# Kernel tuning notes

Hardware: AMD Instinct MI355X
Metric: run time of the kernel (lower is better)

The kernel has to match this reference:

```python
import jax, jax.numpy as jnp
import numpy as np

N_ATOMS = 50000
ATOM_FDIM = 133
HIDDEN = 128
DEPTH = 3
N_EDGES = 800000
N_MOLS = 1024
BN_EPS = 1e-5


def setup_inputs() -> dict:
    key = jax.random.key(0)
    ks = jax.random.split(key, 10)
    f_atoms = jax.random.normal(ks[0], (N_ATOMS, ATOM_FDIM), dtype=jnp.float32)
    W_in = jax.random.normal(ks[1], (ATOM_FDIM, HIDDEN), dtype=jnp.float32) / np.sqrt(ATOM_FDIM)
    b_in = jax.random.normal(ks[2], (HIDDEN,), dtype=jnp.float32) * 0.01
    W1 = jax.random.normal(ks[3], (DEPTH, HIDDEN, HIDDEN), dtype=jnp.float32) / np.sqrt(HIDDEN)
    b1 = jax.random.normal(ks[4], (DEPTH, HIDDEN), dtype=jnp.float32) * 0.01
    W2 = jax.random.normal(ks[5], (DEPTH, HIDDEN, HIDDEN), dtype=jnp.float32) / np.sqrt(HIDDEN)
    b2 = jax.random.normal(ks[6], (DEPTH, HIDDEN), dtype=jnp.float32) * 0.01
    gamma = jnp.ones((DEPTH, HIDDEN), dtype=jnp.float32)
    beta = jnp.zeros((DEPTH, HIDDEN), dtype=jnp.float32)
    eps_param = jnp.zeros((DEPTH,), dtype=jnp.float32)
    edge_index = jax.random.randint(ks[7], (2, N_EDGES), 0, N_ATOMS, dtype=jnp.int64 if jax.config.jax_enable_x64 else jnp.int32).astype(jnp.int32)
    segment_ids = jnp.sort(jax.random.randint(ks[8], (N_ATOMS,), 0, N_MOLS).astype(jnp.int32))
    return {"f_atoms": f_atoms, "W_in": W_in, "b_in": b_in, "W1": W1, "b1": b1,
            "W2": W2, "b2": b2, "gamma": gamma, "beta": beta, "eps_param": eps_param,
            "edge_index": edge_index, "segment_ids": segment_ids}


def _gin_forward(f_atoms, W_in, b_in, W1, b1, W2, b2, gamma, beta, eps_param,
                 edge_index, segment_ids):
    src, tgt = edge_index[0], edge_index[1]
    # input projection + ReLU
    x = jax.nn.relu(f_atoms @ W_in + b_in)  # [N, H]
    for d in range(DEPTH):
        # scatter-add of gathered neighbor features + (1+eps) self term
        agg = jnp.zeros_like(x).at[tgt].add(x[src]) + (1.0 + eps_param[d]) * x
        h = jax.nn.relu(agg @ W1[d] + b1[d])
        h = h @ W2[d] + b2[d]
        # BatchNorm1d (training-mode batch statistics)
        mean = jnp.mean(h, axis=0)
        var = jnp.var(h, axis=0)
        h = gamma[d] * (h - mean) * jax.lax.rsqrt(var + BN_EPS) + beta[d]
        x = jax.nn.relu(h)
    # per-molecule mean pooling (a_scope -> segment mean); empty mols -> zeros
    sums = jax.ops.segment_sum(x, segment_ids, num_segments=N_MOLS)  # [M, H]
    counts = jax.ops.segment_sum(jnp.ones((x.shape[0],), x.dtype), segment_ids,
                                 num_segments=N_MOLS)
    mol_vecs = jnp.where(counts[:, None] > 0, sums / jnp.maximum(counts, 1.0)[:, None], 0.0)
    return mol_vecs


def reference(f_atoms, W_in, b_in, W1, b1, W2, b2, gamma, beta, eps_param,
              edge_index, segment_ids):
    return _gin_forward(f_atoms, W_in, b_in, W1, b1, W2, b2, gamma, beta,
                        eps_param, edge_index, segment_ids)
```

## Files before the change

### kernel.cpp

```cpp
#include <hip/hip_runtime.h>
#include <hip/hip_fp16.h>

#define N_ATOMS   50000
#define ATOM_FDIM 133
#define HIDDEN    128
#define DEPTH     3
#define N_EDGES   800000
#define N_MOLS    1024
#define BN_EPS    1e-5f
#define K_IN_PAD  160

typedef _Float16 f16x8 __attribute__((ext_vector_type(8)));
typedef float    f32x4 __attribute__((ext_vector_type(4)));

struct __align__(8) half4pack { __half2 a, b; };

__global__ void hist_kernel(const int* __restrict__ idx, int n, int* __restrict__ cnt) {
    int i = blockIdx.x * blockDim.x + threadIdx.x;
    if (i < n) atomicAdd(&cnt[idx[i]], 1);
}

__global__ void scan_block_kernel(const int* __restrict__ in, int* __restrict__ out,
                                  int* __restrict__ bsum, int n) {
    __shared__ int buf[256];
    int i = blockIdx.x * 256 + threadIdx.x;
    int v = (i < n) ? in[i] : 0;
    buf[threadIdx.x] = v;
    __syncthreads();
    #pragma unroll
    for (int off = 1; off < 256; off <<= 1) {
        int t = (threadIdx.x >= off) ? buf[threadIdx.x - off] : 0;
        __syncthreads();
        buf[threadIdx.x] += t;
        __syncthreads();
    }
    if (i < n) out[i] = buf[threadIdx.x] - v;
    if (threadIdx.x == 255) bsum[blockIdx.x] = buf[255];
}

__global__ void scan_top_kernel(int* __restrict__ bsum, int nb) {
    __shared__ int buf[256];
    int v = (threadIdx.x < nb) ? bsum[threadIdx.x] : 0;
    buf[threadIdx.x] = v;
    __syncthreads();
    #pragma unroll
    for (int off = 1; off < 256; off <<= 1) {
        int t = (threadIdx.x >= off) ? buf[threadIdx.x - off] : 0;
        __syncthreads();
        buf[threadIdx.x] += t;
        __syncthreads();
    }
    if (threadIdx.x < nb) bsum[threadIdx.x] = buf[threadIdx.x] - v;
}

__global__ void scan_add_kernel(const int* __restrict__ partial, const int* __restrict__ bsum,
                                int* __restrict__ rowptr, int* __restrict__ wcur,
                                int n, int total) {
    int i = blockIdx.x * 256 + threadIdx.x;
    if (i < n) {
        int v = partial[i] + bsum[blockIdx.x];
        rowptr[i] = v;
        wcur[i]   = v;
    }
    if (i == 0) rowptr[n] = total;
}

__global__ void fill_csr_kernel(const int* __restrict__ src, const int* __restrict__ tgt,
                                int n, int* __restrict__ wcur, unsigned short* __restrict__ col) {
    int e = blockIdx.x * blockDim.x + threadIdx.x;
    if (e < n) {
        int t = tgt[e];
        int p = atomicAdd(&wcur[t], 1);
        col[p] = (unsigned short)src[e];
    }
}

__global__ void setup_kernel(const float* __restrict__ f,
                             const float* __restrict__ W_in,
                             const float* __restrict__ W1,
                             const float* __restrict__ W2,
                             const int* __restrict__ seg,
                             __half* __restrict__ Ah, __half* __restrict__ Wt,
                             float* __restrict__ stats, int* __restrict__ moloff)
{
    const int NCH = N_ATOMS * (K_IN_PAD / 4);
    const int NW4 = (128 * K_IN_PAD + 2 * DEPTH * 128 * 128) / 4;
    int i = blockIdx.x * 256 + threadIdx.x;
    if (i < NCH) {
        int row = i / (K_IN_PAD / 4);
        int c4  = (i - row * (K_IN_PAD / 4)) * 4;
        float v[4];
        #pragma unroll
        for (int u = 0; u < 4; ++u) {
            int k = c4 + u;
            v[u] = (k < ATOM_FDIM) ? f[(size_t)row * ATOM_FDIM + k] : 0.f;
        }
        half4pack p;
        p.a = __float22half2_rn(make_float2(v[0], v[1]));
        p.b = __float22half2_rn(make_float2(v[2], v[3]));
        *(half4pack*)&Ah[(size_t)row * K_IN_PAD + c4] = p;
        return;
    }
    int j = i - NCH;
    if (j < NW4) {
        float v[4];
        #pragma unroll
        for (int u = 0; u < 4; ++u) {
            int e = j * 4 + u;
            if (e < 128 * K_IN_PAD) {
                int n = e / K_IN_PAD, k = e - n * K_IN_PAD;
                v[u] = (k < ATOM_FDIM) ? W_in[(size_t)k * 128 + n] : 0.f;
            } else if (e < 128 * K_IN_PAD + DEPTH * 128 * 128) {
                int q = e - 128 * K_IN_PAD;
                int d = q >> 14, r = q & 16383;
                int n = r >> 7, k = r & 127;
                v[u] = W1[((size_t)d * 128 + k) * 128 + n];
            } else {
                int q = e - 128 * K_IN_PAD - DEPTH * 128 * 128;
                int d = q >> 14, r = q & 16383;
                int n = r >> 7, k = r & 127;
                v[u] = W2[((size_t)d * 128 + k) * 128 + n];
            }
        }
        half4pack p;
        p.a = __float22half2_rn(make_float2(v[0], v[1]));
        p.b = __float22half2_rn(make_float2(v[2], v[3]));
        *(half4pack*)&Wt[j * 4] = p;
        return;
    }
    int m = j - NW4;
    if (m < DEPTH * 256) stats[m] = 0.f;
    if (m <= N_MOLS) {
        int lo = 0, hi = N_ATOMS;
        while (lo < hi) {
            int mid = (lo + hi) >> 1;
            if (seg[mid] < m) lo = mid + 1; else hi = mid;
        }
        moloff[m] = lo;
    }
}

#define LDS_S 40

template<bool RELU>
__global__ __launch_bounds__(256, 2) void mfma_gemm(
    const __half* __restrict__ A, const __half* __restrict__ Bt,
    const float* __restrict__ bias, __half* __restrict__ C, int M, int K)
{
    __shared__ __align__(16) __half As[128 * LDS_S];
    __shared__ __align__(16) __half Bs[128 * LDS_S];

    const int t = threadIdx.x;
    const int w = t >> 6, lane = t & 63;
    const int wm = w >> 1, wn = w & 1;
    const int l15 = lane & 15, quad = lane >> 4;
    const int row0 = blockIdx.x * 128;

    f32x4 acc[4][4];
    #pragma unroll
    for (int mt = 0; mt < 4; ++mt)
        #pragma unroll
        for (int nt = 0; nt < 4; ++nt) acc[mt][nt] = (f32x4){0.f, 0.f, 0.f, 0.f};

    for (int k0 = 0; k0 < K; k0 += 32) {
        #pragma unroll
        for (int i = 0; i < 2; ++i) {
            int c = t * 2 + i;
            int r = c >> 2, o = c & 3;
            int row = row0 + r;
            uint4 v = make_uint4(0, 0, 0, 0);
            if (row < M) v = *(const uint4*)&A[(size_t)row * K + k0 + o * 8];
            *(uint4*)&As[r * LDS_S + o * 8] = v;
        }
        #pragma unroll
        for (int i = 0; i < 2; ++i) {
            int c = t * 2 + i;
            int r = c >> 2, o = c & 3;
            uint4 v = *(const uint4*)&Bt[(size_t)r * K + k0 + o * 8];
            *(uint4*)&Bs[r * LDS_S + o * 8] = v;
        }
        __syncthreads();
        f16x8 af[4], bf[4];
        #pragma unroll
        for (int mt = 0; mt < 4; ++mt)
            af[mt] = *(const f16x8*)&As[(wm * 64 + mt * 16 + l15) * LDS_S + quad * 8];
        #pragma unroll
        for (int nt = 0; nt < 4; ++nt)
            bf[nt] = *(const f16x8*)&Bs[(wn * 64 + nt * 16 + l15) * LDS_S + quad * 8];
        #pragma unroll
        for (int mt = 0; mt < 4; ++mt)
            #pragma unroll
            for (int nt = 0; nt < 4; ++nt)
                acc[mt][nt] = __builtin_amdgcn_mfma_f32_16x16x32_f16(af[mt], bf[nt], acc[mt][nt], 0, 0, 0);
        __syncthreads();
    }

    #pragma unroll
    for (int nt = 0; nt < 4; ++nt) {
        int col = wn * 64 + nt * 16 + l15;
        float b = bias[col];
        #pragma unroll
        for (int mt = 0; mt < 4; ++mt) {
            #pragma unroll
            for (int r = 0; r < 4; ++r) {
                int row = row0 + wm * 64 + mt * 16 + quad * 4 + r;
                if (row < M) {
                    float o = acc[mt][nt][r] + b;
                    if (RELU) o = fmaxf(o, 0.f);
                    C[(size_t)row * 128 + col] = __float2half(o);
                }
            }
        }
    }
}

__global__ __launch_bounds__(256, 2) void mlp_fused(
    const __half* __restrict__ A, const __half* __restrict__ B1t,
    const __half* __restrict__ B2t,
    const float* __restrict__ bias1, const float* __restrict__ bias2,
    __half* __restrict__ C, int M,
    float* __restrict__ s1, float* __restrict__ s2)
{
    __shared__ __align__(16) __half As[4 * 128 * LDS_S];
    __shared__ __align__(16) __half Bs[4 * 128 * LDS_S];

    const int t = threadIdx.x;
    const int w = t >> 6, lane = t & 63;
    const int wm = w >> 1, wn = w & 1;
    const int l15 = lane & 15, quad = lane >> 4;
    const int row0 = blockIdx.x * 128;

    f32x4 acc[4][4];
    #pragma unroll
    for (int mt = 0; mt < 4; ++mt)
        #pragma unroll
        for (int nt = 0; nt < 4; ++nt) acc[mt][nt] = (f32x4){0.f, 0.f, 0.f, 0.f};

    #pragma unroll
    for (int i = 0; i < 8; ++i) {
        int c = i * 256 + t;
        int r = c >> 4, o = c & 15;
        int kc = o >> 2, oo = o & 3;
        int row = row0 + r;
        uint4 v = make_uint4(0, 0, 0, 0);
        if (row < M) v = *(const uint4*)&A[(size_t)row * 128 + o * 8];
        *(uint4*)&As[(kc * 128 + r) * LDS_S + oo * 8] = v;
    }
    #pragma unroll
    for (int i = 0; i < 8; ++i) {
        int c = i * 256 + t;
        int r = c >> 4, o = c & 15;
        int kc = o >> 2, oo = o & 3;
        uint4 v = *(const uint4*)&B1t[(size_t)r * 128 + o * 8];
        *(uint4*)&Bs[(kc * 128 + r) * LDS_S + oo * 8] = v;
    }
    __syncthreads();

    #pragma unroll
    for (int kc = 0; kc < 4; ++kc) {
        f16x8 af[4], bf[4];
        #pragma unroll
        for (int mt = 0; mt < 4; ++mt)
            af[mt] = *(const f16x8*)&As[(kc * 128 + wm * 64 + mt * 16 + l15) * LDS_S + quad * 8];
        #pragma unroll
        for (int nt = 0; nt < 4; ++nt)
            bf[nt] = *(const f16x8*)&Bs[(kc * 128 + wn * 64 + nt * 16 + l15) * LDS_S + quad * 8];
        #pragma unroll
        for (int mt = 0; mt < 4; ++mt)
            #pragma unroll
            for (int nt = 0; nt < 4; ++nt)
                acc[mt][nt] = __builtin_amdgcn_mfma_f32_16x16x32_f16(af[mt], bf[nt], acc[mt][nt], 0, 0, 0);
    }
    __syncthreads();

    #pragma unroll
    for (int nt = 0; nt < 4; ++nt) {
        int k = wn * 64 + nt * 16 + l15;
        float b = bias1[k];
        int kc = k >> 5, ko = k & 31;
        #pragma unroll
        for (int mt = 0; mt < 4; ++mt) {
            #pragma unroll
            for (int r = 0; r < 4; ++r) {
                int rl = wm * 64 + mt * 16 + quad * 4 + r;
                float h = fmaxf(acc[mt][nt][r] + b, 0.f);
                As[(kc * 128 + rl) * LDS_S + ko] = __float2half(h);
            }
        }
    }
    #pragma unroll
    for (int i = 0; i < 8; ++i) {
        int c = i * 256 + t;
        int r = c >> 4, o = c & 15;
        int kc = o >> 2, oo = o & 3;
        uint4 v = *(const uint4*)&B2t[(size_t)r * 128 + o * 8];
        *(uint4*)&Bs[(kc * 128 + r) * LDS_S + oo * 8] = v;
    }
    __syncthreads();

    #pragma unroll
    for (int mt = 0; mt < 4; ++mt)
        #pragma unroll
        for (int nt = 0; nt < 4; ++nt) acc[mt][nt] = (f32x4){0.f, 0.f, 0.f, 0.f};
    #pragma unroll
    for (int kc = 0; kc < 4; ++kc) {
        f16x8 af[4], bf[4];
        #pragma unroll
        for (int mt = 0; mt < 4; ++mt)
            af[mt] = *(const f16x8*)&As[(kc * 128 + wm * 64 + mt * 16 + l15) * LDS_S + quad * 8];
        #pragma unroll
        for (int nt = 0; nt < 4; ++nt)
            bf[nt] = *(const f16x8*)&Bs[(kc * 128 + wn * 64 + nt * 16 + l15) * LDS_S + quad * 8];
        #pragma unroll
        for (int mt = 0; mt < 4; ++mt)
            #pragma unroll
            for (int nt = 0; nt < 4; ++nt)
                acc[mt][nt] = __builtin_amdgcn_mfma_f32_16x16x32_f16(af[mt], bf[nt], acc[mt][nt], 0, 0, 0);
    }

    float ps[4] = {0, 0, 0, 0}, pss[4] = {0, 0, 0, 0};
    #pragma unroll
    for (int nt = 0; nt < 4; ++nt) {
        int col = wn * 64 + nt * 16 + l15;
        float b = bias2[col];
        #pragma unroll
        for (int mt = 0; mt < 4; ++mt) {
            #pragma unroll
            for (int r = 0; r < 4; ++r) {
                int row = row0 + wm * 64 + mt * 16 + quad * 4 + r;
                if (row < M) {
                    float o = acc[mt][nt][r] + b;
                    ps[nt] += o;
                    pss[nt] += o * o;
                    C[(size_t)row * 128 + col] = __float2half(o);
                }
            }
        }
    }

    float* red1 = (float*)As;
    float* red2 = (float*)Bs;
    int contrib = wm * 4 + quad;
    __syncthreads();
    #pragma unroll
    for (int nt = 0; nt < 4; ++nt) {
        int col = wn * 64 + nt * 16 + l15;
        red1[contrib * 128 + col] = ps[nt];
        red2[contrib * 128 + col] = pss[nt];
    }
    __syncthreads();
    if (t < 128) {
        float s = 0.f, q = 0.f;
        #pragma unroll
        for (int g = 0; g < 8; ++g) {
            s += red1[g * 128 + t];
            q += red2[g * 128 + t];
        }
        atomicAdd(&s1[t], s);
        atomicAdd(&s2[t], q);
    }
}

template<bool BN>
__global__ __launch_bounds__(256) void aggregate_kernel(
    const __half2* __restrict__ xh2, const int* __restrict__ rowptr,
    const unsigned short* __restrict__ col, const float* __restrict__ eps_param, int d,
    const float* __restrict__ s1, const float* __restrict__ s2,
    const float* __restrict__ gamma, const float* __restrict__ beta, int dprev,
    __half2* __restrict__ aggh2)
{
    int gw = (blockIdx.x * 256 + threadIdx.x) >> 6;
    int lane = threadIdx.x & 63;
    float e1 = 1.0f + eps_param[d];

    float2 sc = make_float2(0.f, 0.f), sh = make_float2(0.f, 0.f);
    if (BN) {
        const float inv_n = 1.0f / (float)N_ATOMS;
        int c0 = lane * 2;
        float m0 = s1[c0] * inv_n;
        float v0 = fmaxf(s2[c0] * inv_n - m0 * m0, 0.f);
        float m1 = s1[c0 + 1] * inv_n;
        float v1 = fmaxf(s2[c0 + 1] * inv_n - m1 * m1, 0.f);
        sc.x = gamma[dprev * 128 + c0]     * rsqrtf(v0 + BN_EPS);
        sc.y = gamma[dprev * 128 + c0 + 1] * rsqrtf(v1 + BN_EPS);
        sh.x = beta[dprev * 128 + c0]     - m0 * sc.x;
        sh.y = beta[dprev * 128 + c0 + 1] - m1 * sc.y;
    }

    float2 a = __half22float2(xh2[(size_t)gw * 64 + lane]);
    if (BN) {
        a.x = fmaxf(a.x * sc.x + sh.x, 0.f);
        a.y = fmaxf(a.y * sc.y + sh.y, 0.f);
    }
    float2 acc;
    acc.x = a.x * e1;
    acc.y = a.y * e1;

    int s = rowptr[gw], e = rowptr[gw + 1];
    for (int i = s; i < e; i += 8) {
        #pragma unroll
        for (int u = 0; u < 8; ++u) {
            int idx = i + u;
            int c = col[min(idx, e - 1)];
            float2 f = __half22float2(xh2[(size_t)c * 64 + lane]);
            if (BN) {
                f.x = fmaxf(f.x * sc.x + sh.x, 0.f);
                f.y = fmaxf(f.y * sc.y + sh.y, 0.f);
            }
            if (idx < e) {
                acc.x += f.x;
                acc.y += f.y;
            }
        }
    }
    aggh2[(size_t)gw * 64 + lane] = __float22half2_rn(acc);
}

__global__ void pool_kernel(const __half* __restrict__ hh, const int* __restrict__ off,
                            const float* __restrict__ s1, const float* __restrict__ s2,
                            const float* __restrict__ gamma, const float* __restrict__ beta,
                            int dprev, float* __restrict__ out)
{
    int m = blockIdx.x;
    int c = threadIdx.x;
    const float inv_n = 1.0f / (float)N_ATOMS;
    float mean = s1[c] * inv_n;
    float var = fmaxf(s2[c] * inv_n - mean * mean, 0.f);
    float sc = gamma[dprev * 128 + c] * rsqrtf(var + BN_EPS);
    float sh = beta[dprev * 128 + c] - mean * sc;
    int s = off[m], e = off[m + 1];
    float acc = 0.f;
    for (int r = s; r < e; ++r) {
        float v = __half2float(hh[(size_t)r * 128 + c]);
        acc += fmaxf(v * sc + sh, 0.f);
    }
    int cnt = e - s;
    out[m * 128 + c] = (cnt > 0) ? acc / (float)cnt : 0.f;
}

extern "C" void kernel_launch(void* const* d_in, const int* in_sizes, int n_in,
                              void* d_out, int out_size, void* d_ws, size_t ws_size,
                              hipStream_t stream)
{
    const float* f_atoms   = (const float*)d_in[0];
    const float* W_in      = (const float*)d_in[1];
    const float* b_in      = (const float*)d_in[2];
    const float* W1        = (const float*)d_in[3];
    const float* b1        = (const float*)d_in[4];
    const float* W2        = (const float*)d_in[5];
    const float* b2        = (const float*)d_in[6];
    const float* gamma     = (const float*)d_in[7];
    const float* beta      = (const float*)d_in[8];
    const float* eps_param = (const float*)d_in[9];
    const int*   edge_index= (const int*)d_in[10];
    const int*   seg       = (const int*)d_in[11];
    const int*   src = edge_index;
    const int*   tgt = edge_index + N_EDGES;
    float* out = (float*)d_out;

    char* ws = (char*)d_ws;
    size_t off = 0;
    auto alloc = [&](size_t bytes) -> char* {
        char* p = ws + off;
        off += (bytes + 255) & ~(size_t)255;
        return p;
    };
    __half* xh    = (__half*)alloc((size_t)N_ATOMS * HIDDEN * 2);
    __half* aggh  = (__half*)alloc((size_t)N_ATOMS * HIDDEN * 2);
    __half* hpre  = (__half*)alloc((size_t)N_ATOMS * HIDDEN * 2);
    __half* Ah    = (__half*)alloc((size_t)N_ATOMS * K_IN_PAD * 2);
    __half* Wt    = (__half*)alloc((size_t)(128 * K_IN_PAD + 2 * DEPTH * 128 * 128) * 2);
    int*   rowptr = (int*)alloc((N_ATOMS + 1) * 4);
    int*   wcur   = (int*)alloc(N_ATOMS * 4);
    int*   partial= (int*)alloc(N_ATOMS * 4);
    int*   bsum   = (int*)alloc(256 * 4);
    unsigned short* col = (unsigned short*)alloc((size_t)N_EDGES * 2);
    float* s12    = (float*)alloc(DEPTH * 256 * 4);
    int*   moloff = (int*)alloc((N_MOLS + 1) * 4);

    const __half* Wt_in = Wt;
    const __half* W1t   = Wt + 128 * K_IN_PAD;
    const __half* W2t   = W1t + DEPTH * 128 * 128;

    hipMemsetAsync(wcur, 0, N_ATOMS * 4, stream);
    hist_kernel<<<(N_EDGES + 255) / 256, 256, 0, stream>>>(tgt, N_EDGES, wcur);
    const int NB = (N_ATOMS + 255) / 256;
    scan_block_kernel<<<NB, 256, 0, stream>>>(wcur, partial, bsum, N_ATOMS);
    scan_top_kernel<<<1, 256, 0, stream>>>(bsum, NB);
    scan_add_kernel<<<NB, 256, 0, stream>>>(partial, bsum, rowptr, wcur, N_ATOMS, N_EDGES);
    fill_csr_kernel<<<(N_EDGES + 255) / 256, 256, 0, stream>>>(src, tgt, N_EDGES, wcur, col);

    {
        const int NCH = N_ATOMS * (K_IN_PAD / 4);
        const int NW4 = (128 * K_IN_PAD + 2 * DEPTH * 128 * 128) / 4;
        const int TOT = NCH + NW4 + N_MOLS + 1;
        setup_kernel<<<(TOT + 255) / 256, 256, 0, stream>>>(
            f_atoms, W_in, W1, W2, seg, Ah, Wt, s12, moloff);
    }

    const int GB = (N_ATOMS + 127) / 128;
    mfma_gemm<true><<<GB, 256, 0, stream>>>(Ah, Wt_in, b_in, xh, N_ATOMS, K_IN_PAD);

    for (int d = 0; d < DEPTH; ++d) {
        float* s1d = s12 + d * 256;
        float* s2d = s1d + 128;
        if (d == 0) {
            aggregate_kernel<false><<<N_ATOMS / 4, 256, 0, stream>>>(
                (const __half2*)xh, rowptr, col, eps_param, d,
                nullptr, nullptr, nullptr, nullptr, 0, (__half2*)aggh);
        } else {
            float* s1p = s12 + (d - 1) * 256;
            float* s2p = s1p + 128;
            aggregate_kernel<true><<<N_ATOMS / 4, 256, 0, stream>>>(
                (const __half2*)hpre, rowptr, col, eps_param, d,
                s1p, s2p, gamma, beta, d - 1, (__half2*)aggh);
        }
        mlp_fused<<<GB, 256, 0, stream>>>(
            aggh, W1t + (size_t)d * 128 * 128, W2t + (size_t)d * 128 * 128,
            b1 + d * HIDDEN, b2 + d * HIDDEN, hpre, N_ATOMS, s1d, s2d);
    }

    pool_kernel<<<N_MOLS, 128, 0, stream>>>(
        hpre, moloff, s12 + (DEPTH - 1) * 256, s12 + (DEPTH - 1) * 256 + 128,
        gamma, beta, DEPTH - 1, out);
}
```

Before: 391.9 us.

## Fuse CSR fill into setup, single-stage input GEMM, packed fp16 aggregation

```diff
diff --git a/kernel.cpp b/kernel.cpp
--- a/kernel.cpp
+++ b/kernel.cpp
@@ -11,6 +11,7 @@
 #define K_IN_PAD  160
 
 typedef _Float16 f16x8 __attribute__((ext_vector_type(8)));
+typedef _Float16 f16x2 __attribute__((ext_vector_type(2)));
 typedef float    f32x4 __attribute__((ext_vector_type(4)));
 
 struct __align__(8) half4pack { __half2 a, b; };
@@ -65,27 +66,27 @@
     if (i == 0) rowptr[n] = total;
 }
 
-__global__ void fill_csr_kernel(const int* __restrict__ src, const int* __restrict__ tgt,
-                                int n, int* __restrict__ wcur, unsigned short* __restrict__ col) {
-    int e = blockIdx.x * blockDim.x + threadIdx.x;
-    if (e < n) {
+#define FB (N_EDGES / 256)
+__global__ void fill_setup_kernel(const int* __restrict__ src, const int* __restrict__ tgt,
+                                  int* __restrict__ wcur, unsigned short* __restrict__ col,
+                                  const float* __restrict__ f,
+                                  const float* __restrict__ W_in,
+                                  const float* __restrict__ W1,
+                                  const float* __restrict__ W2,
+                                  const int* __restrict__ seg,
+                                  __half* __restrict__ Ah, __half* __restrict__ Wt,
+                                  float* __restrict__ stats, int* __restrict__ moloff)
+{
+    if (blockIdx.x < FB) {
+        int e = blockIdx.x * 256 + threadIdx.x;
         int t = tgt[e];
         int p = atomicAdd(&wcur[t], 1);
         col[p] = (unsigned short)src[e];
-    }
-}
-
-__global__ void setup_kernel(const float* __restrict__ f,
-                             const float* __restrict__ W_in,
-                             const float* __restrict__ W1,
-                             const float* __restrict__ W2,
-                             const int* __restrict__ seg,
-                             __half* __restrict__ Ah, __half* __restrict__ Wt,
-                             float* __restrict__ stats, int* __restrict__ moloff)
-{
+        return;
+    }
     const int NCH = N_ATOMS * (K_IN_PAD / 4);
     const int NW4 = (128 * K_IN_PAD + 2 * DEPTH * 128 * 128) / 4;
-    int i = blockIdx.x * 256 + threadIdx.x;
+    int i = (blockIdx.x - FB) * 256 + threadIdx.x;
     if (i < NCH) {
         int row = i / (K_IN_PAD / 4);
         int c4  = (i - row * (K_IN_PAD / 4)) * 4;
@@ -142,13 +143,12 @@
 
 #define LDS_S 40
 
-template<bool RELU>
-__global__ __launch_bounds__(256, 2) void mfma_gemm(
+__global__ __launch_bounds__(256, 2) void mfma_gemm160(
     const __half* __restrict__ A, const __half* __restrict__ Bt,
-    const float* __restrict__ bias, __half* __restrict__ C, int M, int K)
+    const float* __restrict__ bias, __half* __restrict__ C, int M)
 {
-    __shared__ __align__(16) __half As[128 * LDS_S];
-    __shared__ __align__(16) __half Bs[128 * LDS_S];
+    __shared__ __align__(16) __half As[5 * 128 * LDS_S];
+    __shared__ __align__(16) __half Bs[5 * 128 * LDS_S];
 
     const int t = threadIdx.x;
     const int w = t >> 6, lane = t & 63;
@@ -162,37 +162,40 @@
         #pragma unroll
         for (int nt = 0; nt < 4; ++nt) acc[mt][nt] = (f32x4){0.f, 0.f, 0.f, 0.f};
 
-    for (int k0 = 0; k0 < K; k0 += 32) {
-        #pragma unroll
-        for (int i = 0; i < 2; ++i) {
-            int c = t * 2 + i;
-            int r = c >> 2, o = c & 3;
-            int row = row0 + r;
-            uint4 v = make_uint4(0, 0, 0, 0);
-            if (row < M) v = *(const uint4*)&A[(size_t)row * K + k0 + o * 8];
-            *(uint4*)&As[r * LDS_S + o * 8] = v;
-        }
-        #pragma unroll
-        for (int i = 0; i < 2; ++i) {
-            int c = t * 2 + i;
-            int r = c >> 2, o = c & 3;
-            uint4 v = *(const uint4*)&Bt[(size_t)r * K + k0 + o * 8];
-            *(uint4*)&Bs[r * LDS_S + o * 8] = v;
-        }
-        __syncthreads();
+    #pragma unroll
+    for (int i = 0; i < 10; ++i) {
+        int c = i * 256 + t;
+        int r = c / 20, o = c - r * 20;
+        int kc = o >> 2, oo = o & 3;
+        int row = row0 + r;
+        uint4 v = make_uint4(0, 0, 0, 0);
+        if (row < M) v = *(const uint4*)&A[(size_t)row * K_IN_PAD + o * 8];
+        *(uint4*)&As[(kc * 128 + r) * LDS_S + oo * 8] = v;
+    }
+    #pragma unroll
+    for (int i = 0; i < 10; ++i) {
+        int c = i * 256 + t;
+        int r = c / 20, o = c - r * 20;
+        int kc = o >> 2, oo = o & 3;
+        uint4 v = *(const uint4*)&Bt[(size_t)r * K_IN_PAD + o * 8];
+        *(uint4*)&Bs[(kc * 128 + r) * LDS_S + oo * 8] = v;
+    }
+    __syncthreads();
+
+    #pragma unroll
+    for (int kc = 0; kc < 5; ++kc) {
         f16x8 af[4], bf[4];
         #pragma unroll
         for (int mt = 0; mt < 4; ++mt)
-            af[mt] = *(const f16x8*)&As[(wm * 64 + mt * 16 + l15) * LDS_S + quad * 8];
+            af[mt] = *(const f16x8*)&As[(kc * 128 + wm * 64 + mt * 16 + l15) * LDS_S + quad * 8];
         #pragma unroll
         for (int nt = 0; nt < 4; ++nt)
-            bf[nt] = *(const f16x8*)&Bs[(wn * 64 + nt * 16 + l15) * LDS_S + quad * 8];
+            bf[nt] = *(const f16x8*)&Bs[(kc * 128 + wn * 64 + nt * 16 + l15) * LDS_S + quad * 8];
         #pragma unroll
         for (int mt = 0; mt < 4; ++mt)
             #pragma unroll
             for (int nt = 0; nt < 4; ++nt)
                 acc[mt][nt] = __builtin_amdgcn_mfma_f32_16x16x32_f16(af[mt], bf[nt], acc[mt][nt], 0, 0, 0);
-        __syncthreads();
     }
 
     #pragma unroll
@@ -205,8 +208,7 @@
             for (int r = 0; r < 4; ++r) {
                 int row = row0 + wm * 64 + mt * 16 + quad * 4 + r;
                 if (row < M) {
-                    float o = acc[mt][nt][r] + b;
-                    if (RELU) o = fmaxf(o, 0.f);
+                    float o = fmaxf(acc[mt][nt][r] + b, 0.f);
                     C[(size_t)row * 128 + col] = __float2half(o);
                 }
             }
@@ -363,17 +365,18 @@
 
 template<bool BN>
 __global__ __launch_bounds__(256) void aggregate_kernel(
-    const __half2* __restrict__ xh2, const int* __restrict__ rowptr,
+    const f16x2* __restrict__ xh2, const int* __restrict__ rowptr,
     const unsigned short* __restrict__ col, const float* __restrict__ eps_param, int d,
     const float* __restrict__ s1, const float* __restrict__ s2,
     const float* __restrict__ gamma, const float* __restrict__ beta, int dprev,
-    __half2* __restrict__ aggh2)
+    f16x2* __restrict__ aggh2)
 {
     int gw = (blockIdx.x * 256 + threadIdx.x) >> 6;
     int lane = threadIdx.x & 63;
     float e1 = 1.0f + eps_param[d];
 
-    float2 sc = make_float2(0.f, 0.f), sh = make_float2(0.f, 0.f);
+    float sc_x = 1.f, sc_y = 1.f, c_x = 0.f, c_y = 0.f;
+    f16x2 c2 = (f16x2){(_Float16)0.f, (_Float16)0.f};
     if (BN) {
         const float inv_n = 1.0f / (float)N_ATOMS;
         int c0 = lane * 2;
@@ -381,39 +384,62 @@
         float v0 = fmaxf(s2[c0] * inv_n - m0 * m0, 0.f);
         float m1 = s1[c0 + 1] * inv_n;
         float v1 = fmaxf(s2[c0 + 1] * inv_n - m1 * m1, 0.f);
-        sc.x = gamma[dprev * 128 + c0]     * rsqrtf(v0 + BN_EPS);
-        sc.y = gamma[dprev * 128 + c0 + 1] * rsqrtf(v1 + BN_EPS);
-        sh.x = beta[dprev * 128 + c0]     - m0 * sc.x;
-        sh.y = beta[dprev * 128 + c0 + 1] - m1 * sc.y;
-    }
-
-    float2 a = __half22float2(xh2[(size_t)gw * 64 + lane]);
+        sc_x = gamma[dprev * 128 + c0]     * rsqrtf(v0 + BN_EPS);
+        sc_y = gamma[dprev * 128 + c0 + 1] * rsqrtf(v1 + BN_EPS);
+        c_x = beta[dprev * 128 + c0]     / sc_x - m0;
+        c_y = beta[dprev * 128 + c0 + 1] / sc_y - m1;
+        c2 = (f16x2){(_Float16)c_x, (_Float16)c_y};
+    }
+
+    f16x2 ah = xh2[(size_t)gw * 64 + lane];
+    float2 a = make_float2((float)ah.x, (float)ah.y);
     if (BN) {
-        a.x = fmaxf(a.x * sc.x + sh.x, 0.f);
-        a.y = fmaxf(a.y * sc.y + sh.y, 0.f);
+        a.x = sc_x * fmaxf(a.x + c_x, 0.f);
+        a.y = sc_y * fmaxf(a.y + c_y, 0.f);
     }
     float2 acc;
     acc.x = a.x * e1;
     acc.y = a.y * e1;
 
+    const f16x2 z2 = (f16x2){(_Float16)0.f, (_Float16)0.f};
     int s = rowptr[gw], e = rowptr[gw + 1];
-    for (int i = s; i < e; i += 8) {
+    int i = s;
+    for (; i + 8 <= e; i += 8) {
+        f16x2 v[8];
         #pragma unroll
         for (int u = 0; u < 8; ++u) {
-            int idx = i + u;
-            int c = col[min(idx, e - 1)];
-            float2 f = __half22float2(xh2[(size_t)c * 64 + lane]);
-            if (BN) {
-                f.x = fmaxf(f.x * sc.x + sh.x, 0.f);
-                f.y = fmaxf(f.y * sc.y + sh.y, 0.f);
-            }
-            if (idx < e) {
-                acc.x += f.x;
-                acc.y += f.y;
-            }
-        }
-    }
-    aggh2[(size_t)gw * 64 + lane] = __float22half2_rn(acc);
+            int c = col[i + u];
+            v[u] = xh2[(size_t)c * 64 + lane];
+        }
+        if (BN) {
+            #pragma unroll
+            for (int u = 0; u < 8; ++u)
+                v[u] = __builtin_elementwise_max(v[u] + c2, z2);
+        }
+        f16x2 p0 = v[0] + v[1], p1 = v[2] + v[3];
+        f16x2 p2 = v[4] + v[5], p3 = v[6] + v[7];
+        f16x2 q0 = p0 + p1, q1 = p2 + p3;
+        f16x2 r2 = q0 + q1;
+        float frx = (float)r2.x, fry = (float)r2.y;
+        if (BN) {
+            acc.x = fmaf(sc_x, frx, acc.x);
+            acc.y = fmaf(sc_y, fry, acc.y);
+        } else {
+            acc.x += frx;
+            acc.y += fry;
+        }
+    }
+    for (; i < e; ++i) {
+        f16x2 vh = xh2[(size_t)col[i] * 64 + lane];
+        float fx = (float)vh.x, fy = (float)vh.y;
+        if (BN) {
+            fx = sc_x * fmaxf(fx + c_x, 0.f);
+            fy = sc_y * fmaxf(fy + c_y, 0.f);
+        }
+        acc.x += fx;
+        acc.y += fy;
+    }
+    aggh2[(size_t)gw * 64 + lane] = (f16x2){(_Float16)acc.x, (_Float16)acc.y};
 }
 
 __global__ void pool_kernel(const __half* __restrict__ hh, const int* __restrict__ off,
@@ -488,32 +514,31 @@
     scan_block_kernel<<<NB, 256, 0, stream>>>(wcur, partial, bsum, N_ATOMS);
     scan_top_kernel<<<1, 256, 0, stream>>>(bsum, NB);
     scan_add_kernel<<<NB, 256, 0, stream>>>(partial, bsum, rowptr, wcur, N_ATOMS, N_EDGES);
-    fill_csr_kernel<<<(N_EDGES + 255) / 256, 256, 0, stream>>>(src, tgt, N_EDGES, wcur, col);
 
     {
         const int NCH = N_ATOMS * (K_IN_PAD / 4);
         const int NW4 = (128 * K_IN_PAD + 2 * DEPTH * 128 * 128) / 4;
-        const int TOT = NCH + NW4 + N_MOLS + 1;
-        setup_kernel<<<(TOT + 255) / 256, 256, 0, stream>>>(
-            f_atoms, W_in, W1, W2, seg, Ah, Wt, s12, moloff);
+        const int SB  = (NCH + NW4 + N_MOLS + 1 + 255) / 256;
+        fill_setup_kernel<<<FB + SB, 256, 0, stream>>>(
+            src, tgt, wcur, col, f_atoms, W_in, W1, W2, seg, Ah, Wt, s12, moloff);
     }
 
     const int GB = (N_ATOMS + 127) / 128;
-    mfma_gemm<true><<<GB, 256, 0, stream>>>(Ah, Wt_in, b_in, xh, N_ATOMS, K_IN_PAD);
+    mfma_gemm160<<<GB, 256, 0, stream>>>(Ah, Wt_in, b_in, xh, N_ATOMS);
 
     for (int d = 0; d < DEPTH; ++d) {
         float* s1d = s12 + d * 256;
         float* s2d = s1d + 128;
         if (d == 0) {
             aggregate_kernel<false><<<N_ATOMS / 4, 256, 0, stream>>>(
-                (const __half2*)xh, rowptr, col, eps_param, d,
-                nullptr, nullptr, nullptr, nullptr, 0, (__half2*)aggh);
+                (const f16x2*)xh, rowptr, col, eps_param, d,
+                nullptr, nullptr, nullptr, nullptr, 0, (f16x2*)aggh);
         } else {
             float* s1p = s12 + (d - 1) * 256;
             float* s2p = s1p + 128;
             aggregate_kernel<true><<<N_ATOMS / 4, 256, 0, stream>>>(
-                (const __half2*)hpre, rowptr, col, eps_param, d,
-                s1p, s2p, gamma, beta, d - 1, (__half2*)aggh);
+                (const f16x2*)hpre, rowptr, col, eps_param, d,
+                s1p, s2p, gamma, beta, d - 1, (f16x2*)aggh);
         }
         mlp_fused<<<GB, 256, 0, stream>>>(
             aggh, W1t + (size_t)d * 128 * 128, W2t + (size_t)d * 128 * 128,
```

Result: slower. 419.6 us (+7.1%).
